# Kernel tuning notes

Hardware: AMD Instinct MI355X
Metric: run time of the kernel (lower is better)

The kernel has to match this reference:

```python
import jax, jax.numpy as jnp
import numpy as np

DIM = 2560
N_HEAD = 32
HEAD_DIM = 80
ROT_DIM = 32  # head_dim * partial_rotary_factor
INTER = 10240
EPS = 1e-5
BASE = 10000.0


def setup_inputs() -> dict:
    key = jax.random.key(0)
    ks = jax.random.split(key, 12)
    B, S, D, I = 1, 2048, DIM, INTER
    s = lambda k, shape, scale: (jax.random.normal(k, shape, jnp.float32) * scale)
    return {
        "x": s(ks[0], (B, S, D), 1.0),
        "input_pos": jnp.arange(S, dtype=jnp.int32),
        "mask": jnp.tril(jnp.ones((S, S), dtype=bool)),
        "ln_w": jnp.ones((D,), jnp.float32),
        "ln_b": jnp.zeros((D,), jnp.float32),
        "wqkv_w": s(ks[1], (3 * D, D), 0.02),
        "wqkv_b": jnp.zeros((3 * D,), jnp.float32),
        "wo_w": s(ks[2], (D, D), 0.02),
        "wo_b": jnp.zeros((D,), jnp.float32),
        "w1_w": s(ks[3], (I, D), 0.02),
        "w1_b": jnp.zeros((I,), jnp.float32),
        "w2_w": s(ks[4], (D, I), 0.02),
        "w2_b": jnp.zeros((D,), jnp.float32),
    }


def _rope_cos_sin(positions):
    # positions: [S] int; returns cos,sin of shape [S, ROT_DIM]
    inv_freq = 1.0 / (BASE ** (jnp.arange(0, ROT_DIM, 2, dtype=jnp.float32) / ROT_DIM))
    freqs = positions.astype(jnp.float32)[:, None] * inv_freq[None, :]  # [S, ROT/2]
    emb = jnp.concatenate([freqs, freqs], axis=-1)  # [S, ROT]
    return jnp.cos(emb), jnp.sin(emb)


def _rotate_half(t):
    t1, t2 = jnp.split(t, 2, axis=-1)
    return jnp.concatenate([-t2, t1], axis=-1)


def _apply_rope(t, cos, sin):
    # t: [B,H,S,hd]; rotary applied to first ROT_DIM dims (partial rotary)
    t_rot, t_pass = t[..., :ROT_DIM], t[..., ROT_DIM:]
    t_rot = t_rot * cos[None, None] + _rotate_half(t_rot) * sin[None, None]
    return jnp.concatenate([t_rot, t_pass], axis=-1)


def reference(x, input_pos, mask, ln_w, ln_b, wqkv_w, wqkv_b, wo_w, wo_b,
              w1_w, w1_b, w2_w, w2_b):
    B, S, D = x.shape
    H, hd = N_HEAD, HEAD_DIM
    # shared LayerNorm (parallel block)
    mu = jnp.mean(x, axis=-1, keepdims=True)
    var = jnp.mean(jnp.square(x - mu), axis=-1, keepdims=True)
    h = (x - mu) * jax.lax.rsqrt(var + EPS) * ln_w + ln_b

    # fused QKV
    qkv = h @ wqkv_w.T + wqkv_b  # [B,S,3D]
    q, k, v = jnp.split(qkv, 3, axis=-1)
    q = q.reshape(B, S, H, hd).transpose(0, 2, 1, 3)  # [B,H,S,hd]
    k = k.reshape(B, S, H, hd).transpose(0, 2, 1, 3)
    v = v.reshape(B, S, H, hd).transpose(0, 2, 1, 3)

    cos, sin = _rope_cos_sin(input_pos)
    q = _apply_rope(q, cos, sin)
    k = _apply_rope(k, cos, sin)

    # causal attention
    scores = jnp.einsum("bhqd,bhkd->bhqk", q, k) / np.sqrt(hd).astype(np.float32)
    scores = jnp.where(mask[None, None], scores, jnp.float32(-1e9))
    attn = jax.nn.softmax(scores, axis=-1)
    y = jnp.einsum("bhqk,bhkd->bhqd", attn, v)  # [B,H,S,hd]
    y = y.transpose(0, 2, 1, 3).reshape(B, S, D)
    attn_out = y @ wo_w.T + wo_b

    # fused MLP (phi2: gelu_new / tanh approx)
    ffn = jax.nn.gelu(h @ w1_w.T + w1_b, approximate=True) @ w2_w.T + w2_b

    return attn_out + ffn + x
```

## Files before the change

### kernel.cpp

```cpp
#include <hip/hip_runtime.h>
#include <cstdint>

#define S_LEN 2048
#define DMODEL 2560
#define NHEADS 32
#define HDIM 80
#define DINTER 10240

typedef unsigned short u16;
typedef __bf16 bf16x8 __attribute__((ext_vector_type(8)));
typedef float f32x4 __attribute__((ext_vector_type(4)));

__device__ __forceinline__ float us2f(u16 u) {
  return __builtin_bit_cast(float, ((uint32_t)u) << 16);
}
__device__ __forceinline__ u16 f2us(float f) {
  uint32_t x = __builtin_bit_cast(uint32_t, f);
  x += 0x7fffu + ((x >> 16) & 1u);
  return (u16)(x >> 16);
}

typedef __attribute__((address_space(1))) void gas_void;
typedef __attribute__((address_space(3))) void las_void;
__device__ __forceinline__ void gld16(const void* g, void* l) {
  __builtin_amdgcn_global_load_lds((gas_void*)g, (las_void*)l, 16, 0, 0);
}

#define VMW(N) asm volatile("s_waitcnt vmcnt(" #N ")" ::: "memory")
#define BARRIER()                          \
  do {                                     \
    asm volatile("" ::: "memory");         \
    __builtin_amdgcn_s_barrier();          \
    asm volatile("" ::: "memory");         \
  } while (0)

__global__ void f2b_kernel(const float* __restrict__ src, u16* __restrict__ dst) {
  const size_t i = ((size_t)blockIdx.x * 256 + threadIdx.x) * 8;
  const float4 a = *(const float4*)(src + i);
  const float4 b = *(const float4*)(src + i + 4);
  u16 o[8] = {f2us(a.x), f2us(a.y), f2us(a.z), f2us(a.w),
              f2us(b.x), f2us(b.y), f2us(b.z), f2us(b.w)};
  *(uint4*)(dst + i) = *(uint4*)o;
}

__global__ void initout_kernel(const float* __restrict__ x,
                               const float* __restrict__ wo_b,
                               const float* __restrict__ w2_b,
                               float* __restrict__ out) {
  const size_t idx = ((size_t)blockIdx.x * 256 + threadIdx.x) * 4;
  const int c0 = (int)(idx % DMODEL);
  const float4 vx = *(const float4*)(x + idx);
  const float4 b1 = *(const float4*)(wo_b + c0);
  const float4 b2 = *(const float4*)(w2_b + c0);
  float4 vo;
  vo.x = vx.x + b1.x + b2.x;
  vo.y = vx.y + b1.y + b2.y;
  vo.z = vx.z + b1.z + b2.z;
  vo.w = vx.w + b1.w + b2.w;
  *(float4*)(out + idx) = vo;
}

__global__ void ln_kernel(const float* __restrict__ x, const float* __restrict__ w,
                          const float* __restrict__ b, u16* __restrict__ h) {
  const int s = blockIdx.x, tid = threadIdx.x;
  const float* xr = x + (size_t)s * DMODEL;
  float v[10];
  float sum = 0.f, sq = 0.f;
#pragma unroll
  for (int j = 0; j < 10; j++) {
    v[j] = xr[tid + j * 256];
    sum += v[j];
    sq += v[j] * v[j];
  }
#pragma unroll
  for (int o = 32; o > 0; o >>= 1) {
    sum += __shfl_down(sum, o, 64);
    sq += __shfl_down(sq, o, 64);
  }
  __shared__ float red[8];
  const int wave = tid >> 6, lane = tid & 63;
  if (lane == 0) { red[wave] = sum; red[4 + wave] = sq; }
  __syncthreads();
  sum = red[0] + red[1] + red[2] + red[3];
  sq = red[4] + red[5] + red[6] + red[7];
  const float mu = sum * (1.0f / DMODEL);
  const float var = sq * (1.0f / DMODEL) - mu * mu;
  const float rstd = rsqrtf(var + 1e-5f);
  u16* hr = h + (size_t)s * DMODEL;
#pragma unroll
  for (int j = 0; j < 10; j++) {
    const int d = tid + j * 256;
    hr[d] = f2us((v[j] - mu) * rstd * w[d] + b[d]);
  }
}

template <int ACT, int MODE>
__launch_bounds__(512, 2)
__global__ void gemm256(const u16* __restrict__ A, const u16* __restrict__ B,
                        const float* __restrict__ bias, void* __restrict__ Cv,
                        int M, int N, int K) {
  __shared__ __align__(16) u16 lds[4][16384];
  const int tid = threadIdx.x;
  const int w = tid >> 6, lane = tid & 63;
  const int quad = lane >> 4, l15 = lane & 15;
  const int wm = w >> 2, wn = w & 3;

  const int nwg = gridDim.x * gridDim.y;
  const int flat = blockIdx.x + gridDim.x * blockIdx.y;
  const int swz = (flat & 7) * (nwg >> 3) + (flat >> 3);
  const int ntN = N >> 8;
  const int bm = swz / ntN, bn = swz % ntN;

  const int Kc = K / gridDim.z;
  const int k0 = blockIdx.z * Kc;
  const int nk = Kc >> 6;

  const int stgCol = (((lane & 7) ^ ((lane >> 3) & 7)) * 8);
  const u16* Ag = A + ((size_t)bm * 256 + w * 8 + (lane >> 3)) * K + k0 + stgCol;
  const u16* Bg = B + ((size_t)bn * 256 + w * 8 + (lane >> 3)) * K + k0 + stgCol;

  const int q8 = quad * 8;
  const int swz3 = (l15 & 7) * 8;
  const int arow = wm * 64 + l15;
  const int brow = wn * 32 + l15;

#define STG_HALF(MAT, GP, BUF, HF, KT)                                       \
  do {                                                                       \
    gld16((GP) + (size_t)((HF) * 128) * K + (KT) * 64,                       \
          &lds[(BUF) * 2 + (MAT)][(HF) * 8192 + w * 512]);                   \
    gld16((GP) + (size_t)((HF) * 128 + 64) * K + (KT) * 64,                  \
          &lds[(BUF) * 2 + (MAT)][(HF) * 8192 + 4096 + w * 512]);            \
  } while (0)

#define LD_A(BUF, MH)                                                        \
  _Pragma("unroll") for (int mf_ = 0; mf_ < 4; mf_++)                        \
  _Pragma("unroll") for (int kk_ = 0; kk_ < 2; kk_++)                        \
      aF[mf_][kk_] = *(const bf16x8*)&lds[(BUF) * 2]                         \
          [(arow + (MH) * 128 + mf_ * 16) * 64 + ((kk_ * 32 + q8) ^ swz3)];

#define LD_B(DST, BUF, NH)                                                   \
  _Pragma("unroll") for (int nf_ = 0; nf_ < 2; nf_++)                        \
  _Pragma("unroll") for (int kk_ = 0; kk_ < 2; kk_++)                        \
      DST[nf_][kk_] = *(const bf16x8*)&lds[(BUF) * 2 + 1]                    \
          [(brow + (NH) * 128 + nf_ * 16) * 64 + ((kk_ * 32 + q8) ^ swz3)];

#define MFMA_Q(MH, NH, BF)                                                   \
  do {                                                                       \
    __builtin_amdgcn_s_setprio(1);                                           \
    _Pragma("unroll") for (int kk_ = 0; kk_ < 2; kk_++)                      \
    _Pragma("unroll") for (int mf_ = 0; mf_ < 4; mf_++)                      \
    _Pragma("unroll") for (int nf_ = 0; nf_ < 2; nf_++)                      \
        acc[(MH) * 4 + mf_][(NH) * 2 + nf_] =                                \
            __builtin_amdgcn_mfma_f32_16x16x32_bf16(                         \
                aF[mf_][kk_], BF[nf_][kk_],                                  \
                acc[(MH) * 4 + mf_][(NH) * 2 + nf_], 0, 0, 0);               \
    __builtin_amdgcn_s_setprio(0);                                           \
  } while (0)

  f32x4 acc[8][4] = {};
  bf16x8 aF[4][2], bF0[2][2], bF1[2][2];

  STG_HALF(0, Ag, 0, 0, 0);
  STG_HALF(1, Bg, 0, 0, 0);
  STG_HALF(1, Bg, 0, 1, 0);
  STG_HALF(0, Ag, 0, 1, 0);
  STG_HALF(0, Ag, 1, 0, 1);
  VMW(6);
  BARRIER();

  for (int t = 0; t < nk - 2; ++t) {
    const int bc = t & 1, ob = bc ^ 1;
    LD_A(bc, 0);
    LD_B(bF0, bc, 0);
    STG_HALF(1, Bg, ob, 0, t + 1);
    VMW(6);
    BARRIER();
    MFMA_Q(0, 0, bF0);
    BARRIER();
    LD_B(bF1, bc, 1);
    STG_HALF(1, Bg, ob, 1, t + 1);
    VMW(6);
    BARRIER();
    MFMA_Q(0, 1, bF1);
    BARRIER();
    LD_A(bc, 1);
    STG_HALF(0, Ag, ob, 1, t + 1);
    BARRIER();
    MFMA_Q(1, 1, bF1);
    BARRIER();
    STG_HALF(0, Ag, bc, 0, t + 2);
    VMW(6);
    BARRIER();
    MFMA_Q(1, 0, bF0);
    BARRIER();
  }
  {
    const int bc = (nk - 2) & 1, ob = bc ^ 1;
    LD_A(bc, 0);
    LD_B(bF0, bc, 0);
    STG_HALF(1, Bg, ob, 0, nk - 1);
    VMW(6);
    BARRIER();
    MFMA_Q(0, 0, bF0);
    BARRIER();
    LD_B(bF1, bc, 1);
    STG_HALF(1, Bg, ob, 1, nk - 1);
    VMW(6);
    BARRIER();
    MFMA_Q(0, 1, bF1);
    BARRIER();
    LD_A(bc, 1);
    STG_HALF(0, Ag, ob, 1, nk - 1);
    BARRIER();
    MFMA_Q(1, 1, bF1);
    BARRIER();
    VMW(4);
    BARRIER();
    MFMA_Q(1, 0, bF0);
    BARRIER();
  }
  {
    const int bc = (nk - 1) & 1;
    LD_A(bc, 0);
    LD_B(bF0, bc, 0);
    VMW(2);
    BARRIER();
    MFMA_Q(0, 0, bF0);
    BARRIER();
    LD_B(bF1, bc, 1);
    VMW(0);
    BARRIER();
    MFMA_Q(0, 1, bF1);
    BARRIER();
    LD_A(bc, 1);
    BARRIER();
    MFMA_Q(1, 1, bF1);
    MFMA_Q(1, 0, bF0);
  }

#pragma unroll
  for (int nh = 0; nh < 2; nh++)
#pragma unroll
    for (int nf = 0; nf < 2; nf++) {
      const int col = bn * 256 + nh * 128 + wn * 32 + nf * 16 + l15;
      const float bv = (MODE == 0) ? bias[col] : 0.f;
#pragma unroll
      for (int mh = 0; mh < 2; mh++)
#pragma unroll
        for (int mf = 0; mf < 4; mf++) {
          const int row0 = bm * 256 + mh * 128 + wm * 64 + mf * 16 + quad * 4;
#pragma unroll
          for (int r = 0; r < 4; r++) {
            float v = acc[mh * 4 + mf][nh * 2 + nf][r] + bv;
            if (ACT == 1) {
              const float tt = v * (0.7978845608f + 0.0356774081f * v * v);
              v = 0.5f * v * (1.0f + tanhf(tt));
            }
            if (MODE == 0)
              ((u16*)Cv)[(size_t)(row0 + r) * N + col] = f2us(v);
            else
              atomicAdd((float*)Cv + (size_t)(row0 + r) * N + col, v);
          }
        }
    }
#undef STG_HALF
#undef LD_A
#undef LD_B
#undef MFMA_Q
}

__global__ void rope_kernel(u16* __restrict__ qkv, const int* __restrict__ pos) {
  const int idx = blockIdx.x * 256 + threadIdx.x;
  const int i = idx & 15;
  const int which = (idx >> 4) & 1;
  const int hh = (idx >> 5) & 31;
  const int s = idx >> 10;
  const float p = (float)pos[s];
  const float freq = p * expf(-0.57564627324851f * (float)i);
  float sn, c;
  sincosf(freq, &sn, &c);
  u16* base = qkv + (size_t)s * (3 * DMODEL) + which * DMODEL + hh * HDIM + i;
  const float t0 = us2f(base[0]), t1 = us2f(base[16]);
  base[0] = f2us(t0 * c - t1 * sn);
  base[16] = f2us(t1 * c + t0 * sn);
}

__global__ void attn_kernel(const u16* __restrict__ qkv, u16* __restrict__ y) {
  const int qt = (int)gridDim.x - 1 - (int)blockIdx.x;
  const int h = blockIdx.y;
  const int tid = threadIdx.x, wave = tid >> 6, lane = tid & 63;
  const int quad = lane >> 4, l15 = lane & 15;
  const int qbase = qt * 64;

  __shared__ __align__(16) u16 Qs[64 * 104];
  __shared__ __align__(16) u16 Ks[64 * 104];
  __shared__ __align__(16) u16 Vts[80 * 88];
  __shared__ __align__(16) u16 Ps[4][2][16 * 40];

  for (int i = tid; i < 64 * 104; i += 256) { Qs[i] = 0; Ks[i] = 0; }
  __syncthreads();

  {
    const int r = tid >> 2, c = tid & 3;
    const u16* src = qkv + (size_t)(qbase + r) * (3 * DMODEL) + h * HDIM + c * 20;
    u16* dst = Qs + r * 104 + c * 20;
#pragma unroll
    for (int j = 0; j < 5; j++) {
      ushort4 uv = *(const ushort4*)(src + j * 4);
      ushort4 ov;
      ov.x = f2us(us2f(uv.x) * 0.11180339887f);
      ov.y = f2us(us2f(uv.y) * 0.11180339887f);
      ov.z = f2us(us2f(uv.z) * 0.11180339887f);
      ov.w = f2us(us2f(uv.w) * 0.11180339887f);
      *(ushort4*)(dst + j * 4) = ov;
    }
  }

  float m_i[4], l_i[4];
  f32x4 oacc[5] = {};
#pragma unroll
  for (int r = 0; r < 4; r++) { m_i[r] = -1e30f; l_i[r] = 0.f; }

  const int n_iter = qt + 1;
  __syncthreads();

  for (int it = 0; it < n_iter; ++it) {
    const int kc0 = it * 64;
    if (tid < 128) {
      const int r = tid >> 1, c = (tid & 1) * 40;
      const u16* src =
          qkv + (size_t)(kc0 + r) * (3 * DMODEL) + DMODEL + h * HDIM + c;
      u16* dst = Ks + r * 104 + c;
#pragma unroll
      for (int j = 0; j < 10; j++)
        *(ushort4*)(dst + j * 4) = *(const ushort4*)(src + j * 4);
    } else {
      const int u = tid - 128;
      const int r = u >> 1, c0 = (u & 1) * 40;
      const u16* src =
          qkv + (size_t)(kc0 + r) * (3 * DMODEL) + 2 * DMODEL + h * HDIM + c0;
#pragma unroll
      for (int j = 0; j < 10; j++) {
        ushort4 vv = *(const ushort4*)(src + j * 4);
        const int d0 = c0 + j * 4;
        Vts[(d0 + 0) * 88 + r] = vv.x;
        Vts[(d0 + 1) * 88 + r] = vv.y;
        Vts[(d0 + 2) * 88 + r] = vv.z;
        Vts[(d0 + 3) * 88 + r] = vv.w;
      }
    }
    __syncthreads();

    f32x4 st[4] = {};
    bf16x8 aq[3];
#pragma unroll
    for (int ks = 0; ks < 3; ks++)
      aq[ks] = *(const bf16x8*)&Qs[(wave * 16 + l15) * 104 + ks * 32 + quad * 8];
#pragma unroll
    for (int ks = 0; ks < 3; ks++)
#pragma unroll
      for (int t = 0; t < 4; t++) {
        bf16x8 bk = *(const bf16x8*)&Ks[(t * 16 + l15) * 104 + ks * 32 + quad * 8];
        st[t] = __builtin_amdgcn_mfma_f32_16x16x32_bf16(aq[ks], bk, st[t], 0, 0, 0);
      }

    float sv[4][4], mx[4];
#pragma unroll
    for (int r = 0; r < 4; r++) {
      const int qr = qbase + wave * 16 + quad * 4 + r;
#pragma unroll
      for (int t = 0; t < 4; t++) {
        const int kc = kc0 + t * 16 + l15;
        sv[t][r] = (kc <= qr) ? st[t][r] : -1e30f;
      }
      mx[r] = fmaxf(fmaxf(sv[0][r], sv[1][r]), fmaxf(sv[2][r], sv[3][r]));
    }
#pragma unroll
    for (int o = 1; o < 16; o <<= 1)
#pragma unroll
      for (int r = 0; r < 4; r++) mx[r] = fmaxf(mx[r], __shfl_xor(mx[r], o, 64));

    float alpha[4], rs[4];
#pragma unroll
    for (int r = 0; r < 4; r++) {
      const float mnew = fmaxf(m_i[r], mx[r]);
      alpha[r] = __expf(m_i[r] - mnew);
      m_i[r] = mnew;
      const float p0 = __expf(sv[0][r] - mnew);
      const float p1 = __expf(sv[1][r] - mnew);
      const float p2 = __expf(sv[2][r] - mnew);
      const float p3 = __expf(sv[3][r] - mnew);
      rs[r] = (p0 + p1) + (p2 + p3);
      const int ro = (quad * 4 + r) * 40;
      Ps[wave][0][ro + l15] = f2us(p0);
      Ps[wave][0][ro + 16 + l15] = f2us(p1);
      Ps[wave][1][ro + l15] = f2us(p2);
      Ps[wave][1][ro + 16 + l15] = f2us(p3);
    }
#pragma unroll
    for (int o = 1; o < 16; o <<= 1)
#pragma unroll
      for (int r = 0; r < 4; r++) rs[r] += __shfl_xor(rs[r], o, 64);
#pragma unroll
    for (int r = 0; r < 4; r++) l_i[r] = l_i[r] * alpha[r] + rs[r];
#pragma unroll
    for (int dt = 0; dt < 5; dt++)
#pragma unroll
      for (int r = 0; r < 4; r++) oacc[dt][r] *= alpha[r];

    bf16x8 pf0 = *(const bf16x8*)&Ps[wave][0][l15 * 40 + quad * 8];
    bf16x8 pf1 = *(const bf16x8*)&Ps[wave][1][l15 * 40 + quad * 8];
#pragma unroll
    for (int dt = 0; dt < 5; dt++) {
      bf16x8 vf0 = *(const bf16x8*)&Vts[(dt * 16 + l15) * 88 + quad * 8];
      bf16x8 vf1 = *(const bf16x8*)&Vts[(dt * 16 + l15) * 88 + 32 + quad * 8];
      oacc[dt] = __builtin_amdgcn_mfma_f32_16x16x32_bf16(pf0, vf0, oacc[dt], 0, 0, 0);
      oacc[dt] = __builtin_amdgcn_mfma_f32_16x16x32_bf16(pf1, vf1, oacc[dt], 0, 0, 0);
    }
    __syncthreads();
  }

#pragma unroll
  for (int dt = 0; dt < 5; dt++)
#pragma unroll
    for (int r = 0; r < 4; r++) {
      const int row = qbase + wave * 16 + quad * 4 + r;
      y[(size_t)row * DMODEL + h * HDIM + dt * 16 + l15] = f2us(oacc[dt][r] / l_i[r]);
    }
}

extern "C" void kernel_launch(void* const* d_in, const int* in_sizes, int n_in,
                              void* d_out, int out_size, void* d_ws, size_t ws_size,
                              hipStream_t stream) {
  const float* x = (const float*)d_in[0];
  const int* pos = (const int*)d_in[1];
  const float* ln_w = (const float*)d_in[3];
  const float* ln_b = (const float*)d_in[4];
  const float* wqkv_w = (const float*)d_in[5];
  const float* wqkv_b = (const float*)d_in[6];
  const float* wo_w = (const float*)d_in[7];
  const float* wo_b = (const float*)d_in[8];
  const float* w1_w = (const float*)d_in[9];
  const float* w1_b = (const float*)d_in[10];
  const float* w2_w = (const float*)d_in[11];
  const float* w2_b = (const float*)d_in[12];
  float* out = (float*)d_out;

  char* ws = (char*)d_ws;
  u16* wbuf = (u16*)(ws);
  u16* h = (u16*)(ws + 52428800);
  u16* ffn1 = (u16*)(ws + 62914560);
  u16* qkv = (u16*)(ws + 62914560);
  u16* yAtt = (u16*)(ws + 94371840);

  ln_kernel<<<S_LEN, 256, 0, stream>>>(x, ln_w, ln_b, h);
  initout_kernel<<<(S_LEN * DMODEL / 4) / 256, 256, 0, stream>>>(x, wo_b, w2_b, out);

  f2b_kernel<<<(DINTER * DMODEL) / 2048, 256, 0, stream>>>(w1_w, wbuf);
  gemm256<1, 0><<<dim3(DINTER / 256, S_LEN / 256, 1), 512, 0, stream>>>(
      h, wbuf, w1_b, ffn1, S_LEN, DINTER, DMODEL);
  f2b_kernel<<<(DMODEL * DINTER) / 2048, 256, 0, stream>>>(w2_w, wbuf);
  gemm256<0, 2><<<dim3(DMODEL / 256, S_LEN / 256, 5), 512, 0, stream>>>(
      ffn1, wbuf, w2_b, out, S_LEN, DMODEL, DINTER);

  f2b_kernel<<<(3 * DMODEL * DMODEL) / 2048, 256, 0, stream>>>(wqkv_w, wbuf);
  gemm256<0, 0><<<dim3(3 * DMODEL / 256, S_LEN / 256, 1), 512, 0, stream>>>(
      h, wbuf, wqkv_b, qkv, S_LEN, 3 * DMODEL, DMODEL);
  rope_kernel<<<(S_LEN * NHEADS * 2 * 16) / 256, 256, 0, stream>>>(qkv, pos);
  attn_kernel<<<dim3(S_LEN / 64, NHEADS), 256, 0, stream>>>(qkv, yAtt);
  f2b_kernel<<<(DMODEL * DMODEL) / 2048, 256, 0, stream>>>(wo_w, wbuf);
  gemm256<0, 2><<<dim3(DMODEL / 256, S_LEN / 256, 2), 512, 0, stream>>>(
      yAtt, wbuf, wo_b, out, S_LEN, DMODEL, DMODEL);
}
```

Baseline: 973.7 us.

## Restructure GEMM main loop with register-double-buffered fragments and fewer barriers

Rewrites the gemm256 K-loop into one uniform iteration. The A and B fragments for the next tile are loaded from LDS at the end of the current iteration, into separate aH0/aH1/bH0/bH1 register sets. This cuts the barriers per K-tile from eight to two and removes the separate peeled tail blocks. In exchange, global prefetch now runs only one tile ahead and each iteration starts with a full vmcnt(0) wait, so global-load latency may be less hidden. Register pressure also grows with the extra fragment buffers.

```diff
diff --git a/kernel.cpp b/kernel.cpp
--- a/kernel.cpp
+++ b/kernel.cpp
@@ -112,8 +112,8 @@
   const int bm = swz / ntN, bn = swz % ntN;
 
   const int Kc = K / gridDim.z;
-  const int k0 = blockIdx.z * Kc;
-  const int nk = Kc >> 6;
+  const int k0 = Kc * blockIdx.z;
+  const int nt = Kc >> 6;
 
   const int stgCol = (((lane & 7) ^ ((lane >> 3) & 7)) * 8);
   const u16* Ag = A + ((size_t)bm * 256 + w * 8 + (lane >> 3)) * K + k0 + stgCol;
@@ -126,25 +126,25 @@
 
 #define STG_HALF(MAT, GP, BUF, HF, KT)                                       \
   do {                                                                       \
-    gld16((GP) + (size_t)((HF) * 128) * K + (KT) * 64,                       \
+    gld16((GP) + (size_t)((HF) * 128) * K + (size_t)(KT) * 64,               \
           &lds[(BUF) * 2 + (MAT)][(HF) * 8192 + w * 512]);                   \
-    gld16((GP) + (size_t)((HF) * 128 + 64) * K + (KT) * 64,                  \
+    gld16((GP) + (size_t)((HF) * 128 + 64) * K + (size_t)(KT) * 64,          \
           &lds[(BUF) * 2 + (MAT)][(HF) * 8192 + 4096 + w * 512]);            \
   } while (0)
 
-#define LD_A(BUF, MH)                                                        \
+#define LDS_A(DST, BUF, MH)                                                  \
   _Pragma("unroll") for (int mf_ = 0; mf_ < 4; mf_++)                        \
   _Pragma("unroll") for (int kk_ = 0; kk_ < 2; kk_++)                        \
-      aF[mf_][kk_] = *(const bf16x8*)&lds[(BUF) * 2]                         \
+      DST[mf_][kk_] = *(const bf16x8*)&lds[(BUF) * 2]                        \
           [(arow + (MH) * 128 + mf_ * 16) * 64 + ((kk_ * 32 + q8) ^ swz3)];
 
-#define LD_B(DST, BUF, NH)                                                   \
+#define LDS_B(DST, BUF, NH)                                                  \
   _Pragma("unroll") for (int nf_ = 0; nf_ < 2; nf_++)                        \
   _Pragma("unroll") for (int kk_ = 0; kk_ < 2; kk_++)                        \
       DST[nf_][kk_] = *(const bf16x8*)&lds[(BUF) * 2 + 1]                    \
           [(brow + (NH) * 128 + nf_ * 16) * 64 + ((kk_ * 32 + q8) ^ swz3)];
 
-#define MFMA_Q(MH, NH, BF)                                                   \
+#define MFMA_C(MH, NH, AF, BF)                                               \
   do {                                                                       \
     __builtin_amdgcn_s_setprio(1);                                           \
     _Pragma("unroll") for (int kk_ = 0; kk_ < 2; kk_++)                      \
@@ -152,90 +152,46 @@
     _Pragma("unroll") for (int nf_ = 0; nf_ < 2; nf_++)                      \
         acc[(MH) * 4 + mf_][(NH) * 2 + nf_] =                                \
             __builtin_amdgcn_mfma_f32_16x16x32_bf16(                         \
-                aF[mf_][kk_], BF[nf_][kk_],                                  \
+                AF[mf_][kk_], BF[nf_][kk_],                                  \
                 acc[(MH) * 4 + mf_][(NH) * 2 + nf_], 0, 0, 0);               \
     __builtin_amdgcn_s_setprio(0);                                           \
   } while (0)
 
   f32x4 acc[8][4] = {};
-  bf16x8 aF[4][2], bF0[2][2], bF1[2][2];
+  bf16x8 aH0[4][2], aH1[4][2], bH0[2][2], bH1[2][2];
 
   STG_HALF(0, Ag, 0, 0, 0);
   STG_HALF(1, Bg, 0, 0, 0);
   STG_HALF(1, Bg, 0, 1, 0);
   STG_HALF(0, Ag, 0, 1, 0);
-  STG_HALF(0, Ag, 1, 0, 1);
-  VMW(6);
+  VMW(4);
   BARRIER();
-
-  for (int t = 0; t < nk - 2; ++t) {
+  LDS_A(aH0, 0, 0);
+  LDS_B(bH0, 0, 0);
+
+  for (int t = 0; t < nt; ++t) {
     const int bc = t & 1, ob = bc ^ 1;
-    LD_A(bc, 0);
-    LD_B(bF0, bc, 0);
-    STG_HALF(1, Bg, ob, 0, t + 1);
-    VMW(6);
+    const bool more = (t + 1 < nt);
+    VMW(0);
     BARRIER();
-    MFMA_Q(0, 0, bF0);
-    BARRIER();
-    LD_B(bF1, bc, 1);
-    STG_HALF(1, Bg, ob, 1, t + 1);
-    VMW(6);
-    BARRIER();
-    MFMA_Q(0, 1, bF1);
-    BARRIER();
-    LD_A(bc, 1);
-    STG_HALF(0, Ag, ob, 1, t + 1);
-    BARRIER();
-    MFMA_Q(1, 1, bF1);
-    BARRIER();
-    STG_HALF(0, Ag, bc, 0, t + 2);
-    VMW(6);
-    BARRIER();
-    MFMA_Q(1, 0, bF0);
-    BARRIER();
-  }
-  {
-    const int bc = (nk - 2) & 1, ob = bc ^ 1;
-    LD_A(bc, 0);
-    LD_B(bF0, bc, 0);
-    STG_HALF(1, Bg, ob, 0, nk - 1);
-    VMW(6);
-    BARRIER();
-    MFMA_Q(0, 0, bF0);
-    BARRIER();
-    LD_B(bF1, bc, 1);
-    STG_HALF(1, Bg, ob, 1, nk - 1);
-    VMW(6);
-    BARRIER();
-    MFMA_Q(0, 1, bF1);
-    BARRIER();
-    LD_A(bc, 1);
-    STG_HALF(0, Ag, ob, 1, nk - 1);
-    BARRIER();
-    MFMA_Q(1, 1, bF1);
-    BARRIER();
+    if (more) {
+      STG_HALF(0, Ag, ob, 0, t + 1);
+      STG_HALF(1, Bg, ob, 0, t + 1);
+    }
+    LDS_B(bH1, bc, 1);
+    MFMA_C(0, 0, aH0, bH0);
+    if (more) STG_HALF(1, Bg, ob, 1, t + 1);
+    LDS_A(aH1, bc, 1);
+    MFMA_C(0, 1, aH0, bH1);
+    if (more) STG_HALF(0, Ag, ob, 1, t + 1);
+    MFMA_C(1, 1, aH1, bH1);
     VMW(4);
     BARRIER();
-    MFMA_Q(1, 0, bF0);
-    BARRIER();
-  }
-  {
-    const int bc = (nk - 1) & 1;
-    LD_A(bc, 0);
-    LD_B(bF0, bc, 0);
-    VMW(2);
-    BARRIER();
-    MFMA_Q(0, 0, bF0);
-    BARRIER();
-    LD_B(bF1, bc, 1);
-    VMW(0);
-    BARRIER();
-    MFMA_Q(0, 1, bF1);
-    BARRIER();
-    LD_A(bc, 1);
-    BARRIER();
-    MFMA_Q(1, 1, bF1);
-    MFMA_Q(1, 0, bF0);
+    MFMA_C(1, 0, aH1, bH0);
+    if (more) {
+      LDS_A(aH0, ob, 0);
+      LDS_B(bH0, ob, 0);
+    }
   }
 
 #pragma unroll
@@ -264,9 +220,9 @@
         }
     }
 #undef STG_HALF
-#undef LD_A
-#undef LD_B
-#undef MFMA_Q
+#undef LDS_A
+#undef LDS_B
+#undef MFMA_C
 }
 
 __global__ void rope_kernel(u16* __restrict__ qkv, const int* __restrict__ pos) {
```

Result: no change. 976.0 us (+0.2%).
